# Kernel optimization log

Measured on AMD Instinct MI355X. Metric: run time of the kernel, lower is better.

The kernel has to match this reference:

```python
import jax, jax.numpy as jnp
import numpy as np

ALPHA = 0.2  # LeakyReLU negative slope
NEG_INF = -1e9


def setup_inputs() -> dict:
    key = jax.random.key(0)
    k1, k2, k3, k4 = jax.random.split(key, 4)
    B, N, F_in, F_out = 4, 4096, 128, 128
    h = jax.random.normal(k1, (B, N, F_in), dtype=jnp.float32)
    adj = jax.random.randint(k2, (B, N, N), 0, 2, dtype=jnp.int32)
    # Xavier-uniform init matching nn.Linear weights
    limW = np.sqrt(6.0 / (F_in + F_out))
    W = jax.random.uniform(k3, (F_in, F_out), jnp.float32, -limW, limW)
    lima = np.sqrt(6.0 / (2 * F_out + 1))
    a = jax.random.uniform(k4, (2 * F_out,), jnp.float32, -lima, lima)
    return {"h": h, "adj": adj, "W": W, "a": a}


def reference(h, adj, W, a):
    # h: (B, N, F_in), adj: (B, N, N) int, W: (F_in, F_out), a: (2*F_out,)
    F_out = W.shape[1]
    Wh = jnp.einsum("bnf,fo->bno", h, W)  # (B, N, F_out)
    a_i, a_j = a[:F_out], a[F_out:]
    # e_ij = leakyrelu(a . [Wh_i, Wh_j]) = leakyrelu(a_i.Wh_i + a_j.Wh_j)
    si = Wh @ a_i  # (B, N) contribution of destination node i
    sj = Wh @ a_j  # (B, N) contribution of source node j
    e = si[:, :, None] + sj[:, None, :]  # (B, N, N)
    e = jnp.where(e > 0, e, ALPHA * e)  # LeakyReLU
    e = jnp.where(adj > 0, e, NEG_INF)  # masked scores
    attention = jax.nn.softmax(e, axis=-1)  # (B, N, N)
    # dropout is identity in eval mode
    h_prime = jnp.einsum("bij,bjo->bio", attention, Wh)  # (B, N, F_out)
    return jax.nn.elu(h_prime)  # concat=True -> ELU
```

## Files before the change

### kernel.cpp

```cpp
#include <hip/hip_runtime.h>

#define GN 4096
#define GF 128
#define GB 4

typedef __attribute__((ext_vector_type(8))) short short8;
typedef __attribute__((ext_vector_type(4))) float floatx4;

static __device__ __forceinline__ unsigned short f2bf(float x){
  unsigned int u = __float_as_uint(x);
  u += 0x7FFFu + ((u >> 16) & 1u);
  return (unsigned short)(u >> 16);
}

__global__ __launch_bounds__(256)
void gat_prep(const float* __restrict__ h, const float* __restrict__ W,
              const float* __restrict__ a, unsigned short* __restrict__ whB,
              float* __restrict__ si_g, unsigned short* __restrict__ EFh)
{
  __shared__ float hl[16*GF];
  __shared__ float red[2][2][16];
  const int tid = threadIdx.x;
  const int b   = blockIdx.x >> 8;
  const int r0  = (blockIdx.x & 255) << 4;
  const int o = tid & 127, g = tid >> 7;

  const float4* hb4 = (const float4*)(h + ((size_t)(b*GN + r0))*GF);
  ((float4*)hl)[tid]       = hb4[tid];
  ((float4*)hl)[tid + 256] = hb4[tid + 256];
  __syncthreads();

  float acc[8];
  #pragma unroll
  for (int r=0;r<8;++r) acc[r] = 0.f;
  const float* Wp = W + o;
  for (int f4=0; f4<32; ++f4){
    const float w0 = Wp[(f4*4+0)*GF];
    const float w1 = Wp[(f4*4+1)*GF];
    const float w2 = Wp[(f4*4+2)*GF];
    const float w3 = Wp[(f4*4+3)*GF];
    #pragma unroll
    for (int r=0;r<8;++r){
      const float4 h4 = *(const float4*)&hl[((g<<3)+r)*GF + (f4<<2)];
      acc[r] = fmaf(h4.x, w0, acc[r]);
      acc[r] = fmaf(h4.y, w1, acc[r]);
      acc[r] = fmaf(h4.z, w2, acc[r]);
      acc[r] = fmaf(h4.w, w3, acc[r]);
    }
  }

  const float ai = a[o], aj = a[GF + o];
  const int lane = tid & 63, wh = (tid >> 6) & 1;
  #pragma unroll
  for (int r=0;r<8;++r){
    float vi = acc[r]*ai, vj = acc[r]*aj;
    #pragma unroll
    for (int off=32; off; off>>=1){ vi += __shfl_down(vi, off); vj += __shfl_down(vj, off); }
    if (lane == 0){ red[0][wh][(g<<3)+r] = vi; red[1][wh][(g<<3)+r] = vj; }
  }

  unsigned short us[8] __attribute__((aligned(16)));
  #pragma unroll
  for (int r=0;r<8;++r) us[r] = f2bf(acc[r]);
  {
    const int j0 = r0 + (g<<3);
    unsigned short* dst = whB + (((size_t)(b*128 + (j0>>5))*128 + o)<<5) + (j0&31);
    *(uint4*)dst = *(const uint4*)us;
  }

  __syncthreads();
  if (tid < 16){
    si_g[b*GN + r0 + tid] = red[0][0][tid] + red[0][1][tid];
  } else if (tid < 32){
    const int r = tid - 16;
    const float vsj = red[1][0][r] + red[1][1][r];
    EFh[(size_t)b*8192 + r0 + r]        = f2bf(__expf(vsj));
    EFh[(size_t)b*8192 + 4096 + r0 + r] = f2bf(__expf(0.2f*vsj));
  }
}

__global__ __launch_bounds__(256, 2)
void gat_main(const int* __restrict__ adj, const unsigned short* __restrict__ whB,
              const float* __restrict__ si_g, const unsigned short* __restrict__ EFh,
              float* __restrict__ out)
{
  __shared__ __align__(16) char smem[34304];
  unsigned short* sEj = (unsigned short*)smem;
  unsigned long long* bits64 = (unsigned long long*)(smem + 16384);
  float* smemc = (float*)smem;

  const int tid  = threadIdx.x;
  const int wave = tid >> 6, lane = tid & 63;
  const int b  = (blockIdx.x >> 1) & 3;
  const int i0 = ((((blockIdx.x >> 3) << 1) | (blockIdx.x & 1))) << 5;
  const int m = lane & 15, quad = lane >> 4, q8 = quad << 3;
  const int jw = wave << 10, jw32 = wave << 5;

  const int* adjb = adj + ((size_t)(b*GN + i0))*GN + jw + lane;

#define LOADVV(vv_, chunk_) do { \
    _Pragma("unroll") \
    for (int r=0;r<32;++r) vv_[r] = __builtin_nontemporal_load(adjb + ((chunk_)<<6) + (size_t)r*GN); \
  } while(0)

  int vvA[32], vvB[32];
  LOADVV(vvA, 0);
  LOADVV(vvB, 1);

  const float si0 = si_g[(size_t)b*GN + i0 + m];
  const float si1 = si_g[(size_t)b*GN + i0 + 16 + m];
  const float Ri0 = __expf(-0.8f*si0), Ri1 = __expf(-0.8f*si1);
  const unsigned short* lanebase = whB + ((size_t)b<<19) + (m<<5) + q8;

  {
    const uint4* Eg = (const uint4*)(EFh + (size_t)b*8192);
    uint4* sE4 = (uint4*)sEj;
    #pragma unroll
    for (int k=0;k<4;++k) sE4[tid + (k<<8)] = Eg[tid + (k<<8)];
  }

  floatx4 acc0[8], acc1[8];
  #pragma unroll
  for (int c=0;c<8;++c){ acc0[c] = (floatx4){0.f,0.f,0.f,0.f}; acc1[c] = (floatx4){0.f,0.f,0.f,0.f}; }
  floatx4 lf0 = (floatx4){0.f,0.f,0.f,0.f}, lf1 = (floatx4){0.f,0.f,0.f,0.f};
  const short8 ones8 = {0x3F80,0x3F80,0x3F80,0x3F80,0x3F80,0x3F80,0x3F80,0x3F80};

#define BALLOTS(vv_, bufp_) do { \
    unsigned long long* bw = bits64 + (((wave<<1) | (bufp_)) << 5); \
    _Pragma("unroll") \
    for (int r=0;r<32;++r){ \
      const unsigned long long mm = __ballot(vv_[r] > 0); \
      if (lane == 0) bw[r] = mm; \
    } \
    asm volatile("s_waitcnt lgkmcnt(0)" ::: "memory"); \
  } while(0)

#define BCLOAD(Bc_, chunk_) do { \
    const unsigned short* wb = lanebase + ((size_t)(jw32 + ((chunk_)<<1)) << 12); \
    _Pragma("unroll") \
    for (int c=0;c<8;++c) Bc_[c]   = *(const short8*)(wb + (c<<9)); \
    _Pragma("unroll") \
    for (int c=0;c<8;++c) Bc_[8+c] = *(const short8*)(wb + 4096 + (c<<9)); \
  } while(0)

#define COMPUTE(chunk_, bufp_, Bc_) do { \
    const unsigned int* bwp = (const unsigned int*)(bits64 + (((wave<<1) | (bufp_)) << 5)); \
    _Pragma("unroll") \
    for (int t=0;t<2;++t){ \
      const unsigned int sh0 = bwp[(m<<1)|t] >> q8; \
      const unsigned int sh1 = bwp[((m+16)<<1)|t] >> q8; \
      const int jj = jw + ((((chunk_)<<1)|t)<<5) + q8; \
      const short8 Es = *(const short8*)&sEj[jj]; \
      const short8 Fs = *(const short8*)&sEj[4096 + jj]; \
      const unsigned int* Eu = (const unsigned int*)&Es; \
      const unsigned int* Fu = (const unsigned int*)&Fs; \
      unsigned int aw0[4], aw1[4]; \
      _Pragma("unroll") \
      for (int p=0;p<4;++p){ \
        const float E0 = __uint_as_float(Eu[p] << 16); \
        const float E1 = __uint_as_float(Eu[p] & 0xFFFF0000u); \
        const float F0 = __uint_as_float(Fu[p] << 16); \
        const float F1 = __uint_as_float(Fu[p] & 0xFFFF0000u); \
        const float p00 = fmaxf(E0, Ri0*F0), p01 = fmaxf(E1, Ri0*F1); \
        const float p10 = fmaxf(E0, Ri1*F0), p11 = fmaxf(E1, Ri1*F1); \
        unsigned int w0, w1; \
        asm("v_cvt_pk_bf16_f32 %0, %1, %2" : "=v"(w0) : "v"(p00), "v"(p01)); \
        asm("v_cvt_pk_bf16_f32 %0, %1, %2" : "=v"(w1) : "v"(p10), "v"(p11)); \
        const unsigned int k00 = (unsigned int)(((int)(sh0 << (31-2*p))) >> 31); \
        const unsigned int k01 = (unsigned int)(((int)(sh0 << (30-2*p))) >> 31); \
        const unsigned int k10 = (unsigned int)(((int)(sh1 << (31-2*p))) >> 31); \
        const unsigned int k11 = (unsigned int)(((int)(sh1 << (30-2*p))) >> 31); \
        aw0[p] = w0 & ((k00 & 0xFFFFu) | (k01 << 16)); \
        aw1[p] = w1 & ((k10 & 0xFFFFu) | (k11 << 16)); \
      } \
      const short8 af0 = *(const short8*)aw0; \
      const short8 af1 = *(const short8*)aw1; \
      _Pragma("unroll") \
      for (int c=0;c<8;++c){ \
        acc0[c] = __builtin_amdgcn_mfma_f32_16x16x32_bf16(af0, Bc_[(t<<3)+c], acc0[c], 0, 0, 0); \
        acc1[c] = __builtin_amdgcn_mfma_f32_16x16x32_bf16(af1, Bc_[(t<<3)+c], acc1[c], 0, 0, 0); \
      } \
      lf0 = __builtin_amdgcn_mfma_f32_16x16x32_bf16(af0, ones8, lf0, 0, 0, 0); \
      lf1 = __builtin_amdgcn_mfma_f32_16x16x32_bf16(af1, ones8, lf1, 0, 0, 0); \
    } \
  } while(0)

  __syncthreads();

  BALLOTS(vvA, 0);

  #pragma unroll 1
  for (int ci = 0; ci < 7; ++ci){
    const int c0 = ci << 1;
    {
      short8 BcA[16];
      BCLOAD(BcA, c0);
      LOADVV(vvA, c0+2);
      COMPUTE(c0, 0, BcA);
      BALLOTS(vvB, 1);
    }
    {
      short8 BcB[16];
      BCLOAD(BcB, c0+1);
      LOADVV(vvB, c0+3);
      COMPUTE(c0+1, 1, BcB);
      BALLOTS(vvA, 0);
    }
  }
  { short8 BcA[16]; BCLOAD(BcA, 14); COMPUTE(14, 0, BcA); }
  BALLOTS(vvB, 1);
  { short8 BcB[16]; BCLOAD(BcB, 15); COMPUTE(15, 1, BcB); }

#undef COMPUTE
#undef BCLOAD
#undef BALLOTS
#undef LOADVV

  #pragma unroll 1
  for (int g = 0; g < 2; ++g){
    __syncthreads();
    #pragma unroll
    for (int c=0;c<8;++c){
      #pragma unroll
      for (int r=0;r<4;++r){
        const float v = g ? acc1[c][r] : acc0[c][r];
        smemc[(wave*16 + quad*4 + r)*132 + c*16 + m] = v;
      }
    }
    if (m == 0){
      #pragma unroll
      for (int r=0;r<4;++r) smemc[8448 + wave*16 + quad*4 + r] = g ? lf1[r] : lf0[r];
    }
    __syncthreads();

    const int rr = tid >> 5;
    const int c4 = (tid & 31) << 2;
    #pragma unroll
    for (int hh = 0; hh < 2; ++hh){
      const int row = rr + (hh<<3);
      const float l = smemc[8448+row] + smemc[8448+16+row]
                    + smemc[8448+32+row] + smemc[8448+48+row];
      const float rl = __builtin_amdgcn_rcpf(l);
      float4 o4;
      #pragma unroll
      for (int k=0;k<4;++k){
        const int col = c4 + k;
        const float s = smemc[row*132+col] + smemc[(16+row)*132+col]
                      + smemc[(32+row)*132+col] + smemc[(48+row)*132+col];
        float v = s * rl;
        v = v > 0.f ? v : expm1f(v);
        ((float*)&o4)[k] = v;
      }
      *(float4*)&out[((size_t)(b*GN + i0 + (g<<4) + row))*GF + c4] = o4;
    }
  }
}

extern "C" void kernel_launch(void* const* d_in, const int* in_sizes, int n_in,
                              void* d_out, int out_size, void* d_ws, size_t ws_size,
                              hipStream_t stream)
{
  (void)in_sizes; (void)n_in; (void)out_size; (void)ws_size;
  const float* h   = (const float*)d_in[0];
  const int*   adj = (const int*)d_in[1];
  const float* W   = (const float*)d_in[2];
  const float* a   = (const float*)d_in[3];
  float* out = (float*)d_out;

  char* ws = (char*)d_ws;
  unsigned short* whB   = (unsigned short*)ws;
  float*          si    = (float*)(ws + (size_t)4*1024*1024);
  unsigned short* EFh   = (unsigned short*)(ws + (size_t)4*1024*1024 + 64*1024);

  gat_prep<<<GB*GN/16, 256, 0, stream>>>(h, W, a, whB, si, EFh);
  gat_main<<<GB*GN/32, 256, 0, stream>>>(adj, whB, si, EFh, out);
}
```

Before: 404.4 us.

## Load adjacency as int2 with row rotation and permute node order

Result: no change. 397.2 us (median of 2 runs) (-1.8%).

```diff
diff --git a/kernel.cpp b/kernel.cpp
--- a/kernel.cpp
+++ b/kernel.cpp
@@ -6,12 +6,14 @@
 
 typedef __attribute__((ext_vector_type(8))) short short8;
 typedef __attribute__((ext_vector_type(4))) float floatx4;
+typedef __attribute__((ext_vector_type(2))) int intx2;
 
 static __device__ __forceinline__ unsigned short f2bf(float x){
   unsigned int u = __float_as_uint(x);
   u += 0x7FFFu + ((u >> 16) & 1u);
   return (unsigned short)(u >> 16);
 }
+
 
 __global__ __launch_bounds__(256)
 void gat_prep(const float* __restrict__ h, const float* __restrict__ W,
@@ -64,8 +66,12 @@
   for (int r=0;r<8;++r) us[r] = f2bf(acc[r]);
   {
     const int j0 = r0 + (g<<3);
-    unsigned short* dst = whB + (((size_t)(b*128 + (j0>>5))*128 + o)<<5) + (j0&31);
-    *(uint4*)dst = *(const uint4*)us;
+    const int Je = (j0 & ~127) + ((j0 & 127) >> 1);
+    unsigned short ev[4] __attribute__((aligned(8))) = {us[0],us[2],us[4],us[6]};
+    unsigned short od[4] __attribute__((aligned(8))) = {us[1],us[3],us[5],us[7]};
+    unsigned short* d0 = whB + (((size_t)(b*128 + (Je>>5))*128 + o)<<5) + (Je&31);
+    *(uint2*)d0          = *(const uint2*)ev;
+    *(uint2*)(d0 + 8192) = *(const uint2*)od;
   }
 
   __syncthreads();
@@ -73,9 +79,11 @@
     si_g[b*GN + r0 + tid] = red[0][0][tid] + red[0][1][tid];
   } else if (tid < 32){
     const int r = tid - 16;
+    const int jj = r0 + r;
+    const int J  = (jj & ~127) + ((jj & 1) << 6) + ((jj & 127) >> 1);
     const float vsj = red[1][0][r] + red[1][1][r];
-    EFh[(size_t)b*8192 + r0 + r]        = f2bf(__expf(vsj));
-    EFh[(size_t)b*8192 + 4096 + r0 + r] = f2bf(__expf(0.2f*vsj));
+    EFh[(size_t)b*8192 + J]        = f2bf(__expf(vsj));
+    EFh[(size_t)b*8192 + 4096 + J] = f2bf(__expf(0.2f*vsj));
   }
 }
 
@@ -95,17 +103,20 @@
   const int i0 = ((((blockIdx.x >> 3) << 1) | (blockIdx.x & 1))) << 5;
   const int m = lane & 15, quad = lane >> 4, q8 = quad << 3;
   const int jw = wave << 10, jw32 = wave << 5;
-
-  const int* adjb = adj + ((size_t)(b*GN + i0))*GN + jw + lane;
-
-#define LOADVV(vv_, chunk_) do { \
-    _Pragma("unroll") \
-    for (int r=0;r<32;++r) vv_[r] = __builtin_nontemporal_load(adjb + ((chunk_)<<6) + (size_t)r*GN); \
-  } while(0)
-
-  int vvA[32], vvB[32];
-  LOADVV(vvA, 0);
-  LOADVV(vvB, 1);
+  const int rrot = wave << 3;
+
+  const intx2* adjb2 = (const intx2*)(adj + ((size_t)(b*GN + i0))*GN + jw) + lane;
+
+#define LOADVV(vv_, sc_) do { \
+    _Pragma("unroll") \
+    for (int r=0;r<32;++r){ \
+      const int rr = (r + rrot) & 31; \
+      vv_[r] = __builtin_nontemporal_load(adjb2 + ((sc_)<<6) + rr*(GN/2)); \
+    } \
+  } while(0)
+
+  intx2 vv[32];
+  LOADVV(vv, 0);
 
   const float si0 = si_g[(size_t)b*GN + i0 + m];
   const float si1 = si_g[(size_t)b*GN + i0 + 16 + m];
@@ -125,12 +136,14 @@
   floatx4 lf0 = (floatx4){0.f,0.f,0.f,0.f}, lf1 = (floatx4){0.f,0.f,0.f,0.f};
   const short8 ones8 = {0x3F80,0x3F80,0x3F80,0x3F80,0x3F80,0x3F80,0x3F80,0x3F80};
 
-#define BALLOTS(vv_, bufp_) do { \
-    unsigned long long* bw = bits64 + (((wave<<1) | (bufp_)) << 5); \
+#define BALLOTS(vv_, scdst_) do { \
+    unsigned long long* bw = bits64 + (((wave<<1) | ((scdst_)&1)) << 6); \
     _Pragma("unroll") \
     for (int r=0;r<32;++r){ \
-      const unsigned long long mm = __ballot(vv_[r] > 0); \
-      if (lane == 0) bw[r] = mm; \
+      const int rr = (r + rrot) & 31; \
+      const unsigned long long m0 = __ballot(vv_[r].x > 0); \
+      const unsigned long long m1 = __ballot(vv_[r].y > 0); \
+      if (lane == 0){ bw[(rr<<1)] = m0; bw[(rr<<1)|1] = m1; } \
     } \
     asm volatile("s_waitcnt lgkmcnt(0)" ::: "memory"); \
   } while(0)
@@ -143,13 +156,13 @@
     for (int c=0;c<8;++c) Bc_[8+c] = *(const short8*)(wb + 4096 + (c<<9)); \
   } while(0)
 
-#define COMPUTE(chunk_, bufp_, Bc_) do { \
-    const unsigned int* bwp = (const unsigned int*)(bits64 + (((wave<<1) | (bufp_)) << 5)); \
+#define COMPUTE_CH(sc_, k_, Bc_) do { \
+    const unsigned int* bwp = (const unsigned int*)(bits64 + (((wave<<1) | ((sc_)&1)) << 6)); \
     _Pragma("unroll") \
     for (int t=0;t<2;++t){ \
-      const unsigned int sh0 = bwp[(m<<1)|t] >> q8; \
-      const unsigned int sh1 = bwp[((m+16)<<1)|t] >> q8; \
-      const int jj = jw + ((((chunk_)<<1)|t)<<5) + q8; \
+      const unsigned int sh0 = bwp[(m<<2)|((k_)<<1)|t] >> q8; \
+      const unsigned int sh1 = bwp[((m+16)<<2)|((k_)<<1)|t] >> q8; \
+      const int jj = jw + ((sc_)<<7) + ((k_)<<6) + (t<<5) + q8; \
       const short8 Es = *(const short8*)&sEj[jj]; \
       const short8 Fs = *(const short8*)&sEj[4096 + jj]; \
       const unsigned int* Eu = (const unsigned int*)&Es; \
@@ -187,31 +200,27 @@
 
   __syncthreads();
 
-  BALLOTS(vvA, 0);
+  BALLOTS(vv, 0);
 
   #pragma unroll 1
-  for (int ci = 0; ci < 7; ++ci){
-    const int c0 = ci << 1;
+  for (int sc = 0; sc < 7; ++sc){
     {
-      short8 BcA[16];
-      BCLOAD(BcA, c0);
-      LOADVV(vvA, c0+2);
-      COMPUTE(c0, 0, BcA);
-      BALLOTS(vvB, 1);
+      short8 Bc[16];
+      BCLOAD(Bc, (sc<<1));
+      LOADVV(vv, sc+1);
+      COMPUTE_CH(sc, 0, Bc);
     }
     {
-      short8 BcB[16];
-      BCLOAD(BcB, c0+1);
-      LOADVV(vvB, c0+3);
-      COMPUTE(c0+1, 1, BcB);
-      BALLOTS(vvA, 0);
-    }
-  }
-  { short8 BcA[16]; BCLOAD(BcA, 14); COMPUTE(14, 0, BcA); }
-  BALLOTS(vvB, 1);
-  { short8 BcB[16]; BCLOAD(BcB, 15); COMPUTE(15, 1, BcB); }
-
-#undef COMPUTE
+      short8 Bc[16];
+      BCLOAD(Bc, (sc<<1)|1);
+      COMPUTE_CH(sc, 1, Bc);
+    }
+    BALLOTS(vv, sc+1);
+  }
+  { short8 Bc[16]; BCLOAD(Bc, 14); COMPUTE_CH(7, 0, Bc); }
+  { short8 Bc[16]; BCLOAD(Bc, 15); COMPUTE_CH(7, 1, Bc); }
+
+#undef COMPUTE_CH
 #undef BCLOAD
 #undef BALLOTS
 #undef LOADVV
```
